# Optimization experiments

Measured on AMD Instinct MI355X. Metric: run time of the kernel, lower is better.

The kernel has to match this reference:

```python
import jax, jax.numpy as jnp
import numpy as np

B, S, K, N = 2, 512, 4096, 16384

def setup_inputs() -> dict:
    key = jax.random.key(0)
    k1, k2, k3, k4 = jax.random.split(key, 4)
    x = jax.random.normal(k1, (B, S, K), dtype=jnp.float32)
    # int8-valued quantized weight stored as int32 (values in [-128, 127])
    weight_quant = jax.random.randint(k2, (N, K), -128, 128, dtype=jnp.int32)
    # per-output-row scale, positive and away from zero (quantize_weight clamps min=1e-8)
    scale = jax.random.uniform(k3, (N,), dtype=jnp.float32, minval=0.001, maxval=0.02)
    bias = jax.random.normal(k4, (N,), dtype=jnp.float32)
    return {"x": x, "weight_quant": weight_quant, "scale": scale, "bias": bias}

def reference(x, weight_quant, scale, bias):
    # Dequantize: weight[n,k] = float(weight_quant[n,k]) * scale[n]
    weight = weight_quant.astype(jnp.float32) * scale[:, None]  # [N, K]
    # F.linear: x @ weight.T + bias
    return jnp.einsum('bsk,nk->bsn', x, weight) + bias
```

## Files before the change

kernel.cpp:

```cpp
#include <hip/hip_runtime.h>

typedef __attribute__((ext_vector_type(4))) float f32x4;
typedef __attribute__((ext_vector_type(4))) int   i32x4;

static constexpr int Kd = 4096, Nd = 16384, Md = 1024;
static constexpr int BK = 128;
static constexpr int NT = Kd / BK;


__device__ __forceinline__ void gload16(const char* g, char* l) {
    __builtin_amdgcn_global_load_lds(
        (const __attribute__((address_space(1))) void*)g,
        (__attribute__((address_space(3))) void*)l, 16, 0, 0);
}

__device__ __forceinline__ int pack4(int a, int b, int c, int d) {
    return (a & 255) | ((b & 255) << 8) | ((c & 255) << 16) | (d << 24);
}


__global__ __launch_bounds__(256) void convert_w_kernel(
    const int* __restrict__ wq, char* __restrict__ wb) {
    const int total = (Nd / 256) * NT * 4 * 8 * 64;
    int c = blockIdx.x * 256 + threadIdx.x;
    const int stride = gridDim.x * 256;
    for (; c < total; c += stride) {
        const int l   = c & 63;
        const int fid = (c >> 6) & 7;
        const int wn  = (c >> 9) & 3;
        const int kt  = (c >> 11) & 31;
        const int nt  = c >> 16;
        const int j   = fid >> 2, ni = (fid >> 1) & 1, kkb = fid & 1;
        const int lr  = l & 15,   l4 = l >> 4;
        const int n   = nt * 256 + wn * 64 + j * 32 + ni * 16 + lr;
        const int k0  = kt * 128 + kkb * 64 + l4 * 16;
        const int* src = wq + (size_t)n * Kd + k0;
        i32x4 a = *(const i32x4*)(src);
        i32x4 b = *(const i32x4*)(src + 4);
        i32x4 cc = *(const i32x4*)(src + 8);
        i32x4 d = *(const i32x4*)(src + 12);
        i32x4 o;
        o[0] = pack4(a[0], a[1], a[2], a[3]);
        o[1] = pack4(b[0], b[1], b[2], b[3]);
        o[2] = pack4(cc[0], cc[1], cc[2], cc[3]);
        o[3] = pack4(d[0], d[1], d[2], d[3]);
        *((i32x4*)wb + c) = o;
    }
}


__global__ __launch_bounds__(256) void convert_x_kernel(
    const float* __restrict__ x, char* __restrict__ xb, float* __restrict__ xs) {
    const int row = blockIdx.x;
    const int t   = threadIdx.x;
    const float* xr = x + (size_t)row * Kd;

    f32x4 v[4];
    float amax = 0.f;
    #pragma unroll
    for (int i = 0; i < 4; ++i) {
        v[i] = *(const f32x4*)(xr + t * 16 + i * 4);
        #pragma unroll
        for (int j = 0; j < 4; ++j) amax = fmaxf(amax, fabsf(v[i][j]));
    }
    #pragma unroll
    for (int off = 32; off; off >>= 1)
        amax = fmaxf(amax, __shfl_xor(amax, off));
    __shared__ float wmax[4];
    if ((t & 63) == 0) wmax[t >> 6] = amax;
    __syncthreads();
    amax = fmaxf(fmaxf(wmax[0], wmax[1]), fmaxf(wmax[2], wmax[3]));
    amax = fmaxf(amax, 1e-20f);

    const float inv = 127.0f / amax;
    i32x4 o;
    #pragma unroll
    for (int i = 0; i < 4; ++i) {
        int q[4];
        #pragma unroll
        for (int j = 0; j < 4; ++j) {
            int qi = __float2int_rn(v[i][j] * inv);
            qi = qi > 127 ? 127 : (qi < -127 ? -127 : qi);
            q[j] = qi;
        }
        o[i] = pack4(q[0], q[1], q[2], q[3]);
    }
    *(i32x4*)(xb + (size_t)row * Kd + t * 16) = o;
    if (t == 0) xs[row] = amax * (1.0f / 127.0f);
}


#define BARRIER() asm volatile("s_barrier" ::: "memory")
#define SBAR() __builtin_amdgcn_sched_barrier(0)

#define LGKM0_FENCE() do {                                                     \
    asm volatile("s_waitcnt lgkmcnt(0)");                                      \
    __builtin_amdgcn_sched_barrier(0);                                         \
} while (0)

#define VMCNT(n) do {                                                          \
    asm volatile("s_waitcnt vmcnt(" #n ")" ::: "memory");                      \
    __builtin_amdgcn_sched_barrier(0);                                         \
} while (0)

#define STAGE_AFULL(slot, kt) do {                                             \
    _Pragma("unroll")                                                          \
    for (int h_ = 0; h_ < 2; ++h_) {                                           \
        char* lb_ = &LDSA[slot][h_][w * 8][0];                                 \
        gload16(Ab + (aRow0 + h_ * 64) * (size_t)Kd + (kt) * BK + gcol, lb_);  \
        gload16(Ab + (aRow0 + h_ * 64 + 128) * (size_t)Kd + (kt) * BK + gcol,  \
                lb_ + 64 * 128);                                               \
    }                                                                          \
    __builtin_amdgcn_sched_barrier(0);                                         \
} while (0)

#define LOAD_BF(buf, kt, jj) do {                                              \
    const i32x4* p_ = Bfr + (size_t)(kt) * 2048 + wn * 512 + (jj) * 256 + l;   \
    buf[0][0] = p_[0];                                                         \
    buf[0][1] = p_[64];                                                        \
    buf[1][0] = p_[128];                                                       \
    buf[1][1] = p_[192];                                                       \
    __builtin_amdgcn_sched_barrier(0);                                         \
} while (0)

#define READ_A(dst, slot, h) do {                                              \
    const char* lA_ = &LDSA[slot][h][0][0];                                    \
    _Pragma("unroll")                                                          \
    for (int mi = 0; mi < 4; ++mi)                                             \
        _Pragma("unroll")                                                      \
        for (int kk = 0; kk < 2; ++kk) {                                       \
            const int row_ = wm * 64 + mi * 16 + lr;                           \
            const int col_ = (l4 * 16 + kk * 64) ^ xorv;                       \
            dst[mi][kk] = *(const i32x4*)(lA_ + row_ * 128 + col_);            \
        }                                                                      \
} while (0)

#define MFMA_QUAD(h, j, AF, BF) do {                                           \
    __builtin_amdgcn_s_setprio(1);                                             \
    _Pragma("unroll")                                                          \
    for (int mi = 0; mi < 4; ++mi)                                             \
        _Pragma("unroll")                                                      \
        for (int ni = 0; ni < 2; ++ni)                                         \
            _Pragma("unroll")                                                  \
            for (int kk = 0; kk < 2; ++kk)                                     \
                acc[(h) * 4 + mi][(j) * 2 + ni] =                              \
                    __builtin_amdgcn_mfma_i32_16x16x64_i8(                     \
                        AF[mi][kk], BF[ni][kk],                                \
                        acc[(h) * 4 + mi][(j) * 2 + ni], 0, 0, 0);             \
    __builtin_amdgcn_s_setprio(0);                                             \
} while (0)

#define TILE(slot, oslot, BF0USE, BF0NXT, t) do {                              \
    if ((t) + 1 < NT) {                                                        \
        STAGE_AFULL(oslot, (t) + 1);                                           \
        LOAD_BF(BF0NXT, (t) + 1, 0);                                           \
    }                                                                          \
    READ_A(af, slot, 0);                                                       \
    if ((t) + 1 < NT) { VMCNT(12); } else { VMCNT(4); }                        \
    LGKM0_FENCE();                                                             \
    MFMA_QUAD(0, 0, af, BF0USE);                                               \
    if ((t) + 1 < NT) { VMCNT(8); } else { VMCNT(0); }                         \
    MFMA_QUAD(0, 1, af, bf1);                                                  \
    READ_A(af, slot, 1);                                                       \
    LGKM0_FENCE();                                                             \
    MFMA_QUAD(1, 0, af, BF0USE);                                               \
    MFMA_QUAD(1, 1, af, bf1);                                                  \
    if ((t) + 1 < NT) {                                                        \
        LOAD_BF(bf1, (t) + 1, 1);                                              \
        VMCNT(4);                                                              \
    }                                                                          \
    BARRIER();                                                                 \
} while (0)

__global__ __launch_bounds__(512, 2) void gemm8_kernel(
    const char* __restrict__ Ab,
    const char* __restrict__ Bw,
    const float* __restrict__ sw,
    const float* __restrict__ xs,
    const float* __restrict__ bias,
    float* __restrict__ C) {

    __shared__ __align__(16) char LDSA[2][2][128][128];

    const int tid = threadIdx.x;
    const int l   = tid & 63;
    const int w   = tid >> 6;
    const int wm  = w >> 2;
    const int wn  = w & 3;
    const int lr  = l & 15;
    const int l4  = l >> 4;
    const int xorv = (lr & 7) << 4;

    const int orig = blockIdx.x;
    const int work = (orig & 7) * 32 + (orig >> 3);
    const int gm0 = (work & 3) * 256;
    const int gn0 = (work >> 2) * 256;

    const int g_log = (l & 7) ^ ((l >> 3) & 7);
    const int gcol  = g_log * 16;
    const size_t aRow0 = (size_t)(gm0 + w * 8 + (l >> 3));

    const i32x4* Bfr = (const i32x4*)Bw + (size_t)(work >> 2) * 65536;

    i32x4 af[4][2];
    i32x4 bf0a[2][2], bf0b[2][2];
    i32x4 bf1[2][2];

    i32x4 acc[8][4];
    #pragma unroll
    for (int i = 0; i < 8; ++i)
        #pragma unroll
        for (int j = 0; j < 4; ++j) {
            i32x4 z = {0, 0, 0, 0};
            acc[i][j] = z;
        }

    STAGE_AFULL(0, 0);
    LOAD_BF(bf0a, 0, 0);
    LOAD_BF(bf1, 0, 1);
    VMCNT(8);
    BARRIER();

    #pragma unroll 1
    for (int tt = 0; tt < NT / 2; ++tt) {
        TILE(0, 1, bf0a, bf0b, 2 * tt);
        TILE(1, 0, bf0b, bf0a, 2 * tt + 1);
    }

    #pragma unroll
    for (int bj = 0; bj < 4; ++bj) {
        const int gn = gn0 + wn * 64 + bj * 16 + lr;
        const float sc = sw[gn];
        const float bi = bias[gn];
        #pragma unroll
        for (int ai = 0; ai < 8; ++ai) {
            const int gm = gm0 + wm * 128 + ai * 16 + l4 * 4;
            #pragma unroll
            for (int r = 0; r < 4; ++r)
                C[(size_t)(gm + r) * Nd + gn] =
                    (float)acc[ai][bj][r] * (sc * xs[gm + r]) + bi;
        }
    }
}


__global__ __launch_bounds__(256) void naive_kernel(
    const float* __restrict__ x, const int* __restrict__ wq,
    const float* __restrict__ scale, const float* __restrict__ bias,
    float* __restrict__ out) {
    const int n = blockIdx.x * 256 + threadIdx.x;
    const int m = blockIdx.y;
    if (n >= Nd) return;
    const float* xr = x + (size_t)m * Kd;
    const int*   wr = wq + (size_t)n * Kd;
    float s = 0.f;
    for (int k = 0; k < Kd; ++k) s += xr[k] * (float)wr[k];
    out[(size_t)m * Nd + n] = s * scale[n] + bias[n];
}


extern "C" void kernel_launch(void* const* d_in, const int* in_sizes, int n_in,
                              void* d_out, int out_size, void* d_ws, size_t ws_size,
                              hipStream_t stream) {
    const float* x     = (const float*)d_in[0];
    const int*   wq    = (const int*)d_in[1];
    const float* scale = (const float*)d_in[2];
    const float* bias  = (const float*)d_in[3];
    float* out = (float*)d_out;

    const size_t w_bytes = (size_t)Nd * Kd;
    const size_t x_bytes = (size_t)Md * Kd;
    const size_t s_bytes = (size_t)Md * sizeof(float);
    if (ws_size >= w_bytes + x_bytes + s_bytes && d_ws != nullptr) {
        char*  wb = (char*)d_ws;
        char*  xb = wb + w_bytes;
        float* xs = (float*)(xb + x_bytes);
        convert_w_kernel<<<8192, 256, 0, stream>>>(wq, wb);
        convert_x_kernel<<<Md, 256, 0, stream>>>(x, xb, xs);
        gemm8_kernel<<<256, 512, 0, stream>>>(xb, wb, scale, xs, bias, out);
    } else {
        dim3 grid(Nd / 256, Md);
        naive_kernel<<<grid, 256, 0, stream>>>(x, wq, scale, bias, out);
    }
}
```

Before: 144.9 us.

## Fuse int32-to-int8 weight packing into the GEMM main loop

After: 476.8 us. +229.0%, slower.

```diff
diff --git a/kernel.cpp b/kernel.cpp
--- a/kernel.cpp
+++ b/kernel.cpp
@@ -16,36 +16,6 @@
 
 __device__ __forceinline__ int pack4(int a, int b, int c, int d) {
     return (a & 255) | ((b & 255) << 8) | ((c & 255) << 16) | (d << 24);
-}
-
-
-__global__ __launch_bounds__(256) void convert_w_kernel(
-    const int* __restrict__ wq, char* __restrict__ wb) {
-    const int total = (Nd / 256) * NT * 4 * 8 * 64;
-    int c = blockIdx.x * 256 + threadIdx.x;
-    const int stride = gridDim.x * 256;
-    for (; c < total; c += stride) {
-        const int l   = c & 63;
-        const int fid = (c >> 6) & 7;
-        const int wn  = (c >> 9) & 3;
-        const int kt  = (c >> 11) & 31;
-        const int nt  = c >> 16;
-        const int j   = fid >> 2, ni = (fid >> 1) & 1, kkb = fid & 1;
-        const int lr  = l & 15,   l4 = l >> 4;
-        const int n   = nt * 256 + wn * 64 + j * 32 + ni * 16 + lr;
-        const int k0  = kt * 128 + kkb * 64 + l4 * 16;
-        const int* src = wq + (size_t)n * Kd + k0;
-        i32x4 a = *(const i32x4*)(src);
-        i32x4 b = *(const i32x4*)(src + 4);
-        i32x4 cc = *(const i32x4*)(src + 8);
-        i32x4 d = *(const i32x4*)(src + 12);
-        i32x4 o;
-        o[0] = pack4(a[0], a[1], a[2], a[3]);
-        o[1] = pack4(b[0], b[1], b[2], b[3]);
-        o[2] = pack4(cc[0], cc[1], cc[2], cc[3]);
-        o[3] = pack4(d[0], d[1], d[2], d[3]);
-        *((i32x4*)wb + c) = o;
-    }
 }
 
 
@@ -91,7 +61,6 @@
 
 
 #define BARRIER() asm volatile("s_barrier" ::: "memory")
-#define SBAR() __builtin_amdgcn_sched_barrier(0)
 
 #define LGKM0_FENCE() do {                                                     \
     asm volatile("s_waitcnt lgkmcnt(0)");                                      \
@@ -114,13 +83,29 @@
     __builtin_amdgcn_sched_barrier(0);                                         \
 } while (0)
 
-#define LOAD_BF(buf, kt, jj) do {                                              \
-    const i32x4* p_ = Bfr + (size_t)(kt) * 2048 + wn * 512 + (jj) * 256 + l;   \
-    buf[0][0] = p_[0];                                                         \
-    buf[0][1] = p_[64];                                                        \
-    buf[1][0] = p_[128];                                                       \
-    buf[1][1] = p_[192];                                                       \
-    __builtin_amdgcn_sched_barrier(0);                                         \
+#define LOAD_BRAW(j, kt) do {                                                  \
+    _Pragma("unroll")                                                          \
+    for (int ni = 0; ni < 2; ++ni)                                             \
+        _Pragma("unroll")                                                      \
+        for (int kk = 0; kk < 2; ++kk) {                                       \
+            const int off_ = bOff0 + ((j) * 32 + ni * 16) * Kd                 \
+                             + (kt) * BK + kk * 64;                            \
+            _Pragma("unroll")                                                  \
+            for (int i = 0; i < 4; ++i)                                        \
+                raw[ni][kk][i] = *(const i32x4*)(bBase + off_ + i * 4);        \
+        }                                                                      \
+    __builtin_amdgcn_sched_barrier(0);                                         \
+} while (0)
+
+#define PACK_BF(bfp) do {                                                      \
+    _Pragma("unroll")                                                          \
+    for (int ni = 0; ni < 2; ++ni)                                             \
+        _Pragma("unroll")                                                      \
+        for (int kk = 0; kk < 2; ++kk)                                         \
+            _Pragma("unroll")                                                  \
+            for (int i = 0; i < 4; ++i)                                        \
+                bfp[ni][kk][i] = pack4(raw[ni][kk][i][0], raw[ni][kk][i][1],   \
+                                       raw[ni][kk][i][2], raw[ni][kk][i][3]);  \
 } while (0)
 
 #define READ_A(dst, slot, h) do {                                              \
@@ -150,31 +135,28 @@
     __builtin_amdgcn_s_setprio(0);                                             \
 } while (0)
 
-#define TILE(slot, oslot, BF0USE, BF0NXT, t) do {                              \
-    if ((t) + 1 < NT) {                                                        \
-        STAGE_AFULL(oslot, (t) + 1);                                           \
-        LOAD_BF(BF0NXT, (t) + 1, 0);                                           \
-    }                                                                          \
+#define TILE(slot, oslot, t) do {                                              \
     READ_A(af, slot, 0);                                                       \
-    if ((t) + 1 < NT) { VMCNT(12); } else { VMCNT(4); }                        \
+    VMCNT(0);                                               \
+    PACK_BF(bfp1);                                                             \
+    LOAD_BRAW(0, t);                                  \
+    if ((t) + 1 < NT) STAGE_AFULL(oslot, (t) + 1);        \
     LGKM0_FENCE();                                                             \
-    MFMA_QUAD(0, 0, af, BF0USE);                                               \
-    if ((t) + 1 < NT) { VMCNT(8); } else { VMCNT(0); }                         \
-    MFMA_QUAD(0, 1, af, bf1);                                                  \
+    MFMA_QUAD(0, 1, af, bfp1);                                                 \
+    if ((t) + 1 < NT) { VMCNT(4); } else { VMCNT(0); }         \
+    PACK_BF(bfp0);                                                             \
+    MFMA_QUAD(0, 0, af, bfp0);                                                 \
     READ_A(af, slot, 1);                                                       \
     LGKM0_FENCE();                                                             \
-    MFMA_QUAD(1, 0, af, BF0USE);                                               \
-    MFMA_QUAD(1, 1, af, bf1);                                                  \
-    if ((t) + 1 < NT) {                                                        \
-        LOAD_BF(bf1, (t) + 1, 1);                                              \
-        VMCNT(4);                                                              \
-    }                                                                          \
-    BARRIER();                                                                 \
-} while (0)
-
-__global__ __launch_bounds__(512, 2) void gemm8_kernel(
+    MFMA_QUAD(1, 1, af, bfp1);                            \
+    if ((t) + 1 < NT) LOAD_BRAW(1, (t) + 1);  \
+    MFMA_QUAD(1, 0, af, bfp0);                            \
+    if ((t) + 1 < NT) { VMCNT(16); BARRIER(); }     \
+} while (0)
+
+__global__ __launch_bounds__(512, 2) void gemm8f_kernel(
     const char* __restrict__ Ab,
-    const char* __restrict__ Bw,
+    const int*  __restrict__ Wq,
     const float* __restrict__ sw,
     const float* __restrict__ xs,
     const float* __restrict__ bias,
@@ -200,11 +182,12 @@
     const int gcol  = g_log * 16;
     const size_t aRow0 = (size_t)(gm0 + w * 8 + (l >> 3));
 
-    const i32x4* Bfr = (const i32x4*)Bw + (size_t)(work >> 2) * 65536;
+    const int* bBase = Wq + (size_t)gn0 * Kd;
+    const int  bOff0 = (wn * 64 + lr) * Kd + l4 * 16;
 
     i32x4 af[4][2];
-    i32x4 bf0a[2][2], bf0b[2][2];
-    i32x4 bf1[2][2];
+    i32x4 raw[2][2][4];
+    i32x4 bfp0[2][2], bfp1[2][2];
 
     i32x4 acc[8][4];
     #pragma unroll
@@ -216,15 +199,14 @@
         }
 
     STAGE_AFULL(0, 0);
-    LOAD_BF(bf0a, 0, 0);
-    LOAD_BF(bf1, 0, 1);
-    VMCNT(8);
+    LOAD_BRAW(1, 0);
+    VMCNT(16);
     BARRIER();
 
     #pragma unroll 1
     for (int tt = 0; tt < NT / 2; ++tt) {
-        TILE(0, 1, bf0a, bf0b, 2 * tt);
-        TILE(1, 0, bf0b, bf0a, 2 * tt + 1);
+        TILE(0, 1, 2 * tt);
+        TILE(1, 0, 2 * tt + 1);
     }
 
     #pragma unroll
@@ -268,16 +250,13 @@
     const float* bias  = (const float*)d_in[3];
     float* out = (float*)d_out;
 
-    const size_t w_bytes = (size_t)Nd * Kd;
     const size_t x_bytes = (size_t)Md * Kd;
     const size_t s_bytes = (size_t)Md * sizeof(float);
-    if (ws_size >= w_bytes + x_bytes + s_bytes && d_ws != nullptr) {
-        char*  wb = (char*)d_ws;
-        char*  xb = wb + w_bytes;
+    if (ws_size >= x_bytes + s_bytes && d_ws != nullptr) {
+        char*  xb = (char*)d_ws;
         float* xs = (float*)(xb + x_bytes);
-        convert_w_kernel<<<8192, 256, 0, stream>>>(wq, wb);
         convert_x_kernel<<<Md, 256, 0, stream>>>(x, xb, xs);
-        gemm8_kernel<<<256, 512, 0, stream>>>(xb, wb, scale, xs, bias, out);
+        gemm8f_kernel<<<256, 512, 0, stream>>>(xb, wq, scale, xs, bias, out);
     } else {
         dim3 grid(Nd / 256, Md);
         naive_kernel<<<grid, 256, 0, stream>>>(x, wq, scale, bias, out);
```
